# Optimization experiments

Hardware: AMD Instinct MI355X
Metric: run time of the kernel (lower is better)

Reference implementation:

```python
import jax, jax.numpy as jnp
import numpy as np

NS = (50000, 12500, 3125, 800, 200)   # mesh vertex counts per hierarchy level
CS = (3, 16, 32, 64, 128)             # in_channels + out_channels per level
S = 9       # spiral length
K = 4       # nnz per row of pooling transforms
LATENT = 128
B = 32


def setup_inputs() -> dict:
    key = jax.random.key(0)
    ks = iter(jax.random.split(key, 80))
    inp = {"x": jax.random.normal(next(ks), (B, NS[0], 3), jnp.float32)}
    for l in range(4):
        inp["spiral%d" % l] = jax.random.randint(next(ks), (NS[l], S), 0, NS[l], dtype=jnp.int32)
        # down_transform[l]: sparse (NS[l+1], NS[l])
        inp["down_rows%d" % l] = jnp.repeat(jnp.arange(NS[l + 1], dtype=jnp.int32), K)
        inp["down_cols%d" % l] = jax.random.randint(next(ks), (NS[l + 1] * K,), 0, NS[l], dtype=jnp.int32)
        inp["down_vals%d" % l] = jnp.full((NS[l + 1] * K,), 1.0 / K, jnp.float32)
        # up_transform[l]: sparse (NS[l], NS[l+1])
        inp["up_rows%d" % l] = jnp.repeat(jnp.arange(NS[l], dtype=jnp.int32), K)
        inp["up_cols%d" % l] = jax.random.randint(next(ks), (NS[l] * K,), 0, NS[l + 1], dtype=jnp.int32)
        inp["up_vals%d" % l] = jnp.full((NS[l] * K,), 1.0 / K, jnp.float32)
        # encoder SpiralConv weights: Linear(C_in*S -> C_out), stored (in, out)
        inp["enW%d" % l] = jax.random.normal(next(ks), (CS[l] * S, CS[l + 1]), jnp.float32) * 0.05
        inp["enb%d" % l] = jnp.zeros((CS[l + 1],), jnp.float32)
    inp["muW"] = jax.random.normal(next(ks), (NS[4] * CS[4], LATENT), jnp.float32) * 0.02
    inp["mub"] = jnp.zeros((LATENT,), jnp.float32)
    inp["deW0"] = jax.random.normal(next(ks), (LATENT, NS[4] * CS[4]), jnp.float32) * 0.02
    inp["deb0"] = jnp.zeros((NS[4] * CS[4],), jnp.float32)
    dcin = (CS[4], CS[4], CS[3], CS[2])
    dcout = (CS[4], CS[3], CS[2], CS[1])
    for i in range(4):
        inp["dW%d" % i] = jax.random.normal(next(ks), (dcin[i] * S, dcout[i]), jnp.float32) * 0.05
        inp["db%d" % i] = jnp.zeros((dcout[i],), jnp.float32)
    inp["outW"] = jax.random.normal(next(ks), (CS[1] * S, 3), jnp.float32) * 0.05
    inp["outb"] = jnp.zeros((3,), jnp.float32)
    return inp


def _sconv(x, idx, W, b):
    # x: (B, N, C); idx: (N, S) -> gather spiral neighbors, flatten, dense Linear
    g = x[:, idx.reshape(-1), :].reshape(x.shape[0], idx.shape[0], -1)  # (B, N, S*C)
    return g @ W + b


def _pool(x, rows, cols, vals, M):
    # sparse (M, N) transform applied along vertex dim: index_select + scale + scatter_add
    out = jnp.zeros((x.shape[0], M, x.shape[2]), x.dtype)
    return out.at[:, rows].add(x[:, cols] * vals[None, :, None])


def _forward(x, spirals, downs, ups, enWs, enbs, muW, mub, deW0, deb0, dWs, dbs, outW, outb):
    # encode: (SpiralConv -> ELU -> Pool) x4
    h = x
    for l in range(4):
        h = jax.nn.elu(_sconv(h, spirals[l], enWs[l], enbs[l]))
        h = _pool(h, downs[l][0], downs[l][1], downs[l][2], NS[l + 1])
    h = h.reshape(h.shape[0], -1)  # (B, num_vert * C_last)
    mu = jax.nn.sigmoid(h @ muW + mub)  # is_vae=False path: sigmoid(mu), logvar=None
    z = mu
    # decode: Linear -> (Pool -> SpiralConv -> ELU) x4 -> SpiralConv
    d = (z @ deW0 + deb0).reshape(-1, NS[4], CS[4])
    for i in range(4):
        l = 3 - i
        d = _pool(d, ups[l][0], ups[l][1], ups[l][2], NS[l])
        d = jax.nn.elu(_sconv(d, spirals[l], dWs[i], dbs[i]))
    out = _sconv(d, spirals[0], outW, outb)
    return out, z, mu


def reference(x, spiral0, down_rows0, down_cols0, down_vals0, up_rows0, up_cols0, up_vals0, enW0, enb0, spiral1, down_rows1, down_cols1, down_vals1, up_rows1, up_cols1, up_vals1, enW1, enb1, spiral2, down_rows2, down_cols2, down_vals2, up_rows2, up_cols2, up_vals2, enW2, enb2, spiral3, down_rows3, down_cols3, down_vals3, up_rows3, up_cols3, up_vals3, enW3, enb3, muW, mub, deW0, deb0, dW0, db0, dW1, db1, dW2, db2, dW3, db3, outW, outb):
    spirals = [spiral0, spiral1, spiral2, spiral3]
    downs = [(down_rows0, down_cols0, down_vals0), (down_rows1, down_cols1, down_vals1), (down_rows2, down_cols2, down_vals2), (down_rows3, down_cols3, down_vals3)]
    ups = [(up_rows0, up_cols0, up_vals0), (up_rows1, up_cols1, up_vals1), (up_rows2, up_cols2, up_vals2), (up_rows3, up_cols3, up_vals3)]
    return _forward(x, spirals, downs, ups, [enW0, enW1, enW2, enW3], [enb0, enb1, enb2, enb3], muW, mub, deW0, deb0, [dW0, dW1, dW2, dW3], [db0, db1, db2, db3], outW, outb)
```

## Files before the change

### kernel.cpp

```cpp
#include <hip/hip_runtime.h>
#include <hip/hip_bf16.h>
#include <math.h>

#define NS0 50000
#define NS1 12500
#define NS2 3125
#define NS3 800
#define NS4 200
#define BATCH 32
#define SLEN 9

typedef __hip_bfloat16 bf16;
typedef __attribute__((ext_vector_type(8))) short short8_t;
typedef __attribute__((ext_vector_type(4))) float f32x4;

struct WcvAll {
    const float* W[9];
    bf16* dst[9];
    int K[9], CO[9], KP[9];
    int off[10];
};

__global__ void __launch_bounds__(256)
wconv_all_kernel(WcvAll p)
{
    int gid = blockIdx.x * 256 + threadIdx.x;
    if (gid >= p.off[9]) return;
    int seg = 0;
    #pragma unroll
    for (int s = 1; s < 9; ++s) seg += (gid >= p.off[s]);
    int local = gid - p.off[seg];
    int NKK = p.KP[seg] >> 5;
    int jj   = local & 7;
    int g8   = local >> 3;
    int lane = g8 & 63;
    int blk  = g8 >> 6;
    int kk   = blk % NKK;
    int cb   = blk / NKK;
    int col0 = lane & 15, kh = lane >> 4;
    int co = cb * 16 + col0;
    int k  = kk * 32 + kh * 8 + jj;
    float v = (k < p.K[seg] && co < p.CO[seg]) ? p.W[seg][k * p.CO[seg] + co] : 0.f;
    p.dst[seg][local] = __float2bfloat16(v);
}

__global__ void __launch_bounds__(256)
xpose_in_kernel(const float* __restrict__ x, bf16* __restrict__ xT)
{
    __shared__ short ldsb[256 * 3];
    const int t = threadIdx.x;
    const int n0 = blockIdx.x * 8;
    const int b = t >> 3, v = t & 7;
    const float* src = x + ((size_t)b * NS0 + n0 + v) * 3;
    short* d = &ldsb[(v * 32 + b) * 3];
    d[0] = __bfloat16_as_short(__float2bfloat16(src[0]));
    d[1] = __bfloat16_as_short(__float2bfloat16(src[1]));
    d[2] = __bfloat16_as_short(__float2bfloat16(src[2]));
    __syncthreads();
    short* dst = (short*)xT + ((size_t)n0 * 32 + t) * 3;
    dst[0] = ldsb[t * 3 + 0];
    dst[1] = ldsb[t * 3 + 1];
    dst[2] = ldsb[t * 3 + 2];
}

__global__ void __launch_bounds__(256)
xpose_out_kernel(const float* __restrict__ vm, float* __restrict__ out)
{
    __shared__ float ldsf[256 * 3];
    const int t = threadIdx.x;
    const int n0 = blockIdx.x * 8;
    const float* src = vm + ((size_t)n0 * 32 + t) * 3;
    ldsf[t * 3 + 0] = src[0];
    ldsf[t * 3 + 1] = src[1];
    ldsf[t * 3 + 2] = src[2];
    __syncthreads();
    const int b = t >> 3, v = t & 7;
    float* dst = out + ((size_t)b * NS0 + n0 + v) * 3;
    const float* s = &ldsf[(v * 32 + b) * 3];
    dst[0] = s[0];
    dst[1] = s[1];
    dst[2] = s[2];
}

__global__ void __launch_bounds__(256)
sconv_enc0(const bf16* __restrict__ xT, const int* __restrict__ idx,
           const bf16* __restrict__ Wfrag, const float* __restrict__ bias,
           bf16* __restrict__ y)
{
    __shared__ short lds[64 * 40];
    const int t = threadIdx.x;
    const int n0 = blockIdx.x * 2;

    for (int e = t; e < 64 * 5; e += 256) {
        int r = e / 5, k = 27 + (e - r * 5);
        lds[r * 40 + k] = 0;
    }
    for (int e = t; e < 2 * 9 * 32; e += 256) {
        int v = e / 288;
        int rem = e - v * 288;
        int s = rem >> 5, b = rem & 31;
        int j = idx[(n0 + v) * 9 + s];
        const short* src = (const short*)(xT + (size_t)j * 96 + b * 3);
        short* dst = &lds[(v * 32 + b) * 40 + s * 3];
        dst[0] = src[0];
        dst[1] = src[1];
        dst[2] = src[2];
    }
    __syncthreads();

    const int w = t >> 6, lane = t & 63;
    const int col0 = lane & 15, kh = lane >> 4;
    const int rbase = w * 16;
    float bv = bias[col0];
    f32x4 acc = (f32x4){bv, bv, bv, bv};
    short8_t bfr = *(const short8_t*)(Wfrag + (size_t)lane * 8);
    short8_t afr = *(const short8_t*)&lds[(rbase + col0) * 40 + kh * 8];
    acc = __builtin_amdgcn_mfma_f32_16x16x32_bf16(afr, bfr, acc, 0, 0, 0);
    #pragma unroll
    for (int i = 0; i < 4; ++i) {
        int rl = rbase + kh * 4 + i;
        float v = acc[i];
        v = v > 0.f ? v : expm1f(v);
        y[((size_t)n0 * 32 + rl) * 16 + col0] = __float2bfloat16(v);
    }
}

template<int CIN, int COUT, int COP, int ACT, int NN, typename TOUT>
__global__ void
__launch_bounds__(256, (((9 * CIN + 31) / 32 * 32 / 32) <= 9) ? 4 : 2)
sconv_vm(const bf16* __restrict__ x, const int* __restrict__ idx,
         const bf16* __restrict__ Wfrag, const float* __restrict__ bias,
         TOUT* __restrict__ y)
{
    constexpr int KP  = (9 * CIN + 31) / 32 * 32;
    constexpr int NKK = KP / 32;
    constexpr int NCB = COP / 16;
    constexpr int CH  = (NKK <= 9) ? NKK : 6;
    constexpr int NCHUNK = NKK / CH;
    constexpr int NBUF = (NCHUNK > 1) ? 2 : 1;

    const int t = threadIdx.x, w = t >> 6, lane = t & 63;
    const int n = blockIdx.x * 4 + w;
    if (n >= NN) return;
    const int col0 = lane & 15, kh = lane >> 4;

    int jn[9];
    #pragma unroll
    for (int s = 0; s < 9; ++s) jn[s] = idx[n * 9 + s];

    f32x4 acc[2][NCB];
    #pragma unroll
    for (int cb = 0; cb < NCB; ++cb) {
        int col = cb * 16 + col0;
        float bv = (col < COUT) ? bias[col] : 0.f;
        acc[0][cb] = (f32x4){bv, bv, bv, bv};
        acc[1][cb] = (f32x4){bv, bv, bv, bv};
    }

    const short8_t z8 = {0, 0, 0, 0, 0, 0, 0, 0};
    auto loadA = [&](int kk, short8_t& a0, short8_t& a1) {
        a0 = z8; a1 = z8;
        if constexpr (CIN == 16) {
            const int hi = kh >> 1;
            const int ch = (kh & 1) * 8;
            if (kk < 4) {
                int j = hi ? jn[2 * kk + 1] : jn[2 * kk];
                const bf16* base = x + (size_t)j * 512 + ch;
                a0 = *(const short8_t*)(base + col0 * 16);
                a1 = *(const short8_t*)(base + 256 + col0 * 16);
            } else if (!hi) {
                int j = jn[8];
                const bf16* base = x + (size_t)j * 512 + ch;
                a0 = *(const short8_t*)(base + col0 * 16);
                a1 = *(const short8_t*)(base + 256 + col0 * 16);
            }
        } else {
            constexpr int SPK = CIN / 32;
            const int j = jn[kk / SPK];
            const int ch = (kk % SPK) * 32 + kh * 8;
            const bf16* base = x + (size_t)j * (32 * CIN) + ch;
            a0 = *(const short8_t*)(base + col0 * CIN);
            a1 = *(const short8_t*)(base + (16 + col0) * CIN);
        }
    };

    short8_t bufA[NBUF][2 * CH];
    #pragma unroll
    for (int q = 0; q < CH; ++q)
        loadA(q, bufA[0][2 * q], bufA[0][2 * q + 1]);

    #pragma unroll
    for (int c = 0; c < NCHUNK; ++c) {
        const int cur = (NBUF > 1) ? (c & 1) : 0;
        if (c + 1 < NCHUNK) {
            const int nxt = (NBUF > 1) ? ((c + 1) & 1) : 0;
            #pragma unroll
            for (int q = 0; q < CH; ++q)
                loadA((c + 1) * CH + q, bufA[nxt][2 * q], bufA[nxt][2 * q + 1]);
        }
        #pragma unroll
        for (int q = 0; q < CH; ++q) {
            const int kk = c * CH + q;
            #pragma unroll
            for (int cb = 0; cb < NCB; ++cb) {
                short8_t bfr = *(const short8_t*)(Wfrag + ((size_t)(cb * NKK + kk) * 64 + lane) * 8);
                acc[0][cb] = __builtin_amdgcn_mfma_f32_16x16x32_bf16(bufA[cur][2 * q],     bfr, acc[0][cb], 0, 0, 0);
                acc[1][cb] = __builtin_amdgcn_mfma_f32_16x16x32_bf16(bufA[cur][2 * q + 1], bfr, acc[1][cb], 0, 0, 0);
            }
        }
    }

    #pragma unroll
    for (int f = 0; f < 2; ++f) {
        #pragma unroll
        for (int cb = 0; cb < NCB; ++cb) {
            int col = cb * 16 + col0;
            if (col < COUT) {
                #pragma unroll
                for (int i = 0; i < 4; ++i) {
                    int b = f * 16 + kh * 4 + i;
                    float v = acc[f][cb][i];
                    if (ACT) v = v > 0.f ? v : expm1f(v);
                    TOUT* dst = &y[((size_t)n * 32 + b) * COUT + col];
                    if constexpr (__is_same(TOUT, float)) *dst = v;
                    else *dst = __float2bfloat16(v);
                }
            }
        }
    }
}

template<int C8>
__global__ void __launch_bounds__(256)
pool_vm(const bf16* __restrict__ x, const int* __restrict__ cols,
        const float* __restrict__ vals, bf16* __restrict__ y, int M)
{
    constexpr int BC8 = 32 * C8;
    int tid = blockIdx.x * 256 + threadIdx.x;
    if (tid >= M * BC8) return;
    int m = tid / BC8;
    int e = tid - m * BC8;
    const uint4* xv = (const uint4*)x;
    float acc[8];
    #pragma unroll
    for (int q = 0; q < 8; ++q) acc[q] = 0.f;
    #pragma unroll
    for (int j = 0; j < 4; ++j) {
        int col = cols[m * 4 + j];
        float v = vals[m * 4 + j];
        uint4 u = xv[(size_t)col * BC8 + e];
        const bf16* hh = (const bf16*)&u;
        #pragma unroll
        for (int q = 0; q < 8; ++q)
            acc[q] = fmaf(v, __bfloat162float(hh[q]), acc[q]);
    }
    uint4 o;
    bf16* oh = (bf16*)&o;
    #pragma unroll
    for (int q = 0; q < 8; ++q) oh[q] = __float2bfloat16(acc[q]);
    ((uint4*)y)[(size_t)m * BC8 + e] = o;
}

__global__ void __launch_bounds__(256)
mu_partial_kernel(const bf16* __restrict__ h, const float* __restrict__ W,
                  float* __restrict__ partial)
{
    __shared__ float hs[4096];
    const int t = threadIdx.x;
    const int nb = blockIdx.x;
    const bf16* hb = h + (size_t)nb * 4096;
    for (int e = t; e < 512; e += 256) {
        short8_t v = *(const short8_t*)(hb + e * 8);
        #pragma unroll
        for (int q = 0; q < 8; ++q)
            hs[e * 8 + q] = __bfloat162float(((const bf16*)&v)[q]);
    }
    __syncthreads();
    const int co = t & 127;
    const int bh = t >> 7;
    float acc[16];
    #pragma unroll
    for (int i = 0; i < 16; ++i) acc[i] = 0.f;
    const int k0 = nb * 128;
    for (int k = 0; k < 128; ++k) {
        float wv = W[(size_t)(k0 + k) * 128 + co];
        #pragma unroll
        for (int i = 0; i < 16; ++i)
            acc[i] = fmaf(hs[(bh * 16 + i) * 128 + k], wv, acc[i]);
    }
    float* pb = partial + (size_t)nb * 4096;
    #pragma unroll
    for (int i = 0; i < 16; ++i)
        pb[(bh * 16 + i) * 128 + co] = acc[i];
}

__global__ void __launch_bounds__(256)
mu_reduce_kernel(const float* __restrict__ partial, const float* __restrict__ bias,
                 float* __restrict__ z, float* __restrict__ out_z,
                 float* __restrict__ out_mu)
{
    const int i = blockIdx.x * 256 + threadIdx.x;
    const int co = i & 127;
    float a0 = 0.f, a1 = 0.f, a2 = 0.f, a3 = 0.f;
    #pragma unroll 4
    for (int c = 0; c < 200; c += 4) {
        a0 += partial[(size_t)c * 4096 + i];
        a1 += partial[(size_t)(c + 1) * 4096 + i];
        a2 += partial[(size_t)(c + 2) * 4096 + i];
        a3 += partial[(size_t)(c + 3) * 4096 + i];
    }
    float acc = (a0 + a1) + (a2 + a3) + bias[co];
    float m = 1.f / (1.f + expf(-acc));
    z[i] = m;
    out_z[i] = m;
    out_mu[i] = m;
}

__global__ void __launch_bounds__(256)
de0_kernel(const float* __restrict__ z, const float* __restrict__ W,
           const float* __restrict__ bias, bf16* __restrict__ d)
{
    __shared__ float zs[BATCH * 128];
    const int t = threadIdx.x;
    for (int e = t; e < BATCH * 128; e += 256) zs[e] = z[e];
    __syncthreads();
    const int j = blockIdx.x * 256 + t;
    float bj = bias[j];
    float acc[BATCH];
    #pragma unroll
    for (int b = 0; b < BATCH; ++b) acc[b] = bj;
    for (int k = 0; k < 128; ++k) {
        float w = W[k * 25600 + j];
        #pragma unroll
        for (int b = 0; b < BATCH; ++b)
            acc[b] = fmaf(zs[b * 128 + k], w, acc[b]);
    }
    const int nn = j >> 7, c = j & 127;
    #pragma unroll
    for (int b = 0; b < BATCH; ++b)
        d[(size_t)nn * 4096 + b * 128 + c] = __float2bfloat16(acc[b]);
}

extern "C" void kernel_launch(void* const* d_in, const int* in_sizes, int n_in,
                              void* d_out, int out_size, void* d_ws, size_t ws_size,
                              hipStream_t stream)
{
    const float* x = (const float*)d_in[0];
    const int*   sp[4];
    const int*   dn_cols[4];
    const float* dn_vals[4];
    const int*   up_cols[4];
    const float* up_vals[4];
    const float* enW[4];
    const float* enb[4];
    for (int l = 0; l < 4; ++l) {
        int base = 1 + 9 * l;
        sp[l]      = (const int*)d_in[base + 0];
        dn_cols[l] = (const int*)d_in[base + 2];
        dn_vals[l] = (const float*)d_in[base + 3];
        up_cols[l] = (const int*)d_in[base + 5];
        up_vals[l] = (const float*)d_in[base + 6];
        enW[l]     = (const float*)d_in[base + 7];
        enb[l]     = (const float*)d_in[base + 8];
    }
    const float* muW  = (const float*)d_in[37];
    const float* mub  = (const float*)d_in[38];
    const float* deW0 = (const float*)d_in[39];
    const float* deb0 = (const float*)d_in[40];
    const float* dW[4]  = { (const float*)d_in[41], (const float*)d_in[43],
                            (const float*)d_in[45], (const float*)d_in[47] };
    const float* db[4]  = { (const float*)d_in[42], (const float*)d_in[44],
                            (const float*)d_in[46], (const float*)d_in[48] };
    const float* outW = (const float*)d_in[49];
    const float* outb = (const float*)d_in[50];

    char* ws = (char*)d_ws;
    bf16*  A  = (bf16*)ws;
    bf16*  Bb = (bf16*)(ws + 51200000);
    bf16*  xT = (bf16*)(ws + 51200000);
    float* outVM = (float*)(ws + 51200000);
    float* Z  = (float*)(ws + 153600000);
    bf16*  wEN0 = (bf16*)(ws + 153600000 + 16384);
    bf16*  wOUT = wEN0 + 512;

    float* outF   = (float*)d_out;
    float* out_z  = outF + 4800000;
    float* out_mu = outF + 4804096;

    bf16*  wsc  = (bf16*)d_out;
    bf16*  wEN1 = wsc;
    bf16*  wEN2 = wsc + 5120;
    bf16*  wEN3 = wsc + 23552;
    bf16*  wDW0 = wsc + 97280;
    bf16*  wDW1 = wsc + 244736;
    bf16*  wDW2 = wsc + 318464;
    bf16*  wDW3 = wsc + 336896;
    float* muPart = outF + 1000000;

    WcvAll wp;
    const float* srcs[9] = {enW[0], enW[1], enW[2], enW[3], dW[0], dW[1], dW[2], dW[3], outW};
    bf16* dsts[9] = {wEN0, wEN1, wEN2, wEN3, wDW0, wDW1, wDW2, wDW3, wOUT};
    int Ks[9]   = {27, 144, 288, 576, 1152, 1152, 576, 288, 144};
    int COs[9]  = {16, 32, 64, 128, 128, 64, 32, 16, 3};
    int KPs[9]  = {32, 160, 288, 576, 1152, 1152, 576, 288, 160};
    int COPs[9] = {16, 32, 64, 128, 128, 64, 32, 16, 16};
    int off = 0;
    for (int s = 0; s < 9; ++s) {
        wp.W[s] = srcs[s]; wp.dst[s] = dsts[s];
        wp.K[s] = Ks[s]; wp.CO[s] = COs[s]; wp.KP[s] = KPs[s];
        wp.off[s] = off; off += COPs[s] * KPs[s];
    }
    wp.off[9] = off;
    auto cdiv = [](int a, int b) { return (a + b - 1) / b; };
    wconv_all_kernel<<<cdiv(off, 256), 256, 0, stream>>>(wp);

    xpose_in_kernel<<<NS0 / 8, 256, 0, stream>>>(x, xT);

    sconv_enc0<<<NS0 / 2, 256, 0, stream>>>(xT, sp[0], wEN0, enb[0], A);
    pool_vm<2><<<cdiv(NS1 * 64, 256), 256, 0, stream>>>(A, dn_cols[0], dn_vals[0], Bb, NS1);
    sconv_vm<16, 32, 32, 1, NS1, bf16><<<cdiv(NS1, 4), 256, 0, stream>>>(Bb, sp[1], wEN1, enb[1], A);
    pool_vm<4><<<cdiv(NS2 * 128, 256), 256, 0, stream>>>(A, dn_cols[1], dn_vals[1], Bb, NS2);
    sconv_vm<32, 64, 64, 1, NS2, bf16><<<cdiv(NS2, 4), 256, 0, stream>>>(Bb, sp[2], wEN2, enb[2], A);
    pool_vm<8><<<cdiv(NS3 * 256, 256), 256, 0, stream>>>(A, dn_cols[2], dn_vals[2], Bb, NS3);
    sconv_vm<64, 128, 128, 1, NS3, bf16><<<cdiv(NS3, 4), 256, 0, stream>>>(Bb, sp[3], wEN3, enb[3], A);
    pool_vm<16><<<cdiv(NS4 * 512, 256), 256, 0, stream>>>(A, dn_cols[3], dn_vals[3], Bb, NS4);

    mu_partial_kernel<<<200, 256, 0, stream>>>(Bb, muW, muPart);
    mu_reduce_kernel<<<16, 256, 0, stream>>>(muPart, mub, Z, out_z, out_mu);
    de0_kernel<<<25600 / 256, 256, 0, stream>>>(Z, deW0, deb0, A);

    pool_vm<16><<<cdiv(NS3 * 512, 256), 256, 0, stream>>>(A, up_cols[3], up_vals[3], Bb, NS3);
    sconv_vm<128, 128, 128, 1, NS3, bf16><<<cdiv(NS3, 4), 256, 0, stream>>>(Bb, sp[3], wDW0, db[0], A);
    pool_vm<16><<<cdiv(NS2 * 512, 256), 256, 0, stream>>>(A, up_cols[2], up_vals[2], Bb, NS2);
    sconv_vm<128, 64, 64, 1, NS2, bf16><<<cdiv(NS2, 4), 256, 0, stream>>>(Bb, sp[2], wDW1, db[1], A);
    pool_vm<8><<<cdiv(NS1 * 256, 256), 256, 0, stream>>>(A, up_cols[1], up_vals[1], Bb, NS1);
    sconv_vm<64, 32, 32, 1, NS1, bf16><<<cdiv(NS1, 4), 256, 0, stream>>>(Bb, sp[1], wDW2, db[2], A);
    pool_vm<4><<<cdiv(NS0 * 128, 256), 256, 0, stream>>>(A, up_cols[0], up_vals[0], Bb, NS0);
    sconv_vm<32, 16, 16, 1, NS0, bf16><<<cdiv(NS0, 4), 256, 0, stream>>>(Bb, sp[0], wDW3, db[3], A);

    sconv_vm<16, 3, 16, 0, NS0, float><<<cdiv(NS0, 4), 256, 0, stream>>>(A, sp[0], wOUT, outb, outVM);
    xpose_out_kernel<<<NS0 / 8, 256, 0, stream>>>(outVM, outF);
}
```

Before: 756.7 us.

## Fuse output transpose into final spiral conv and split sconv into small/big variants

The final 3-channel spiral conv now writes directly in batch-major layout through an LDS transpose, removing the separate transpose kernel and its intermediate buffer. The generic sconv kernel is split in two. The small-input variant loads all A fragments before issuing MFMAs. The large-input variant loads each 9-step chunk and then computes, behind a scheduling barrier, replacing the previous double-buffered prefetch. This trades load/compute overlap for lower register pressure and simpler scheduling.

New measurement: 746.0 us. No clear change (-1.4%).

```diff
diff --git a/kernel.cpp b/kernel.cpp
--- a/kernel.cpp
+++ b/kernel.cpp
@@ -64,25 +64,6 @@
 }
 
 __global__ void __launch_bounds__(256)
-xpose_out_kernel(const float* __restrict__ vm, float* __restrict__ out)
-{
-    __shared__ float ldsf[256 * 3];
-    const int t = threadIdx.x;
-    const int n0 = blockIdx.x * 8;
-    const float* src = vm + ((size_t)n0 * 32 + t) * 3;
-    ldsf[t * 3 + 0] = src[0];
-    ldsf[t * 3 + 1] = src[1];
-    ldsf[t * 3 + 2] = src[2];
-    __syncthreads();
-    const int b = t >> 3, v = t & 7;
-    float* dst = out + ((size_t)b * NS0 + n0 + v) * 3;
-    const float* s = &ldsf[(v * 32 + b) * 3];
-    dst[0] = s[0];
-    dst[1] = s[1];
-    dst[2] = s[2];
-}
-
-__global__ void __launch_bounds__(256)
 sconv_enc0(const bf16* __restrict__ xT, const int* __restrict__ idx,
            const bf16* __restrict__ Wfrag, const float* __restrict__ bias,
            bf16* __restrict__ y)
@@ -125,19 +106,17 @@
     }
 }
 
-template<int CIN, int COUT, int COP, int ACT, int NN, typename TOUT>
-__global__ void
-__launch_bounds__(256, (((9 * CIN + 31) / 32 * 32 / 32) <= 9) ? 4 : 2)
-sconv_vm(const bf16* __restrict__ x, const int* __restrict__ idx,
-         const bf16* __restrict__ Wfrag, const float* __restrict__ bias,
-         TOUT* __restrict__ y)
+template<int CIN, int COUT, int COP, int ACT, int NN, int XPOSE, typename TOUT>
+__global__ void __launch_bounds__(256, 4)
+sconv_small(const bf16* __restrict__ x, const int* __restrict__ idx,
+            const bf16* __restrict__ Wfrag, const float* __restrict__ bias,
+            TOUT* __restrict__ y)
 {
     constexpr int KP  = (9 * CIN + 31) / 32 * 32;
     constexpr int NKK = KP / 32;
     constexpr int NCB = COP / 16;
-    constexpr int CH  = (NKK <= 9) ? NKK : 6;
-    constexpr int NCHUNK = NKK / CH;
-    constexpr int NBUF = (NCHUNK > 1) ? 2 : 1;
+    constexpr int XD  = XPOSE ? 4 : 1;
+    __shared__ float xls[XD][32][3];
 
     const int t = threadIdx.x, w = t >> 6, lane = t & 63;
     const int n = blockIdx.x * 4 + w;
@@ -158,8 +137,10 @@
     }
 
     const short8_t z8 = {0, 0, 0, 0, 0, 0, 0, 0};
-    auto loadA = [&](int kk, short8_t& a0, short8_t& a1) {
-        a0 = z8; a1 = z8;
+    short8_t fa[2 * NKK];
+    #pragma unroll
+    for (int kk = 0; kk < NKK; ++kk) {
+        short8_t a0 = z8, a1 = z8;
         if constexpr (CIN == 16) {
             const int hi = kh >> 1;
             const int ch = (kh & 1) * 8;
@@ -175,37 +156,113 @@
                 a1 = *(const short8_t*)(base + 256 + col0 * 16);
             }
         } else {
-            constexpr int SPK = CIN / 32;
+            const int j = jn[kk];
+            const bf16* base = x + (size_t)j * 1024 + kh * 8;
+            a0 = *(const short8_t*)(base + col0 * 32);
+            a1 = *(const short8_t*)(base + (16 + col0) * 32);
+        }
+        fa[2 * kk] = a0;
+        fa[2 * kk + 1] = a1;
+    }
+    __builtin_amdgcn_sched_barrier(0);
+
+    #pragma unroll
+    for (int kk = 0; kk < NKK; ++kk) {
+        #pragma unroll
+        for (int cb = 0; cb < NCB; ++cb) {
+            short8_t bfr = *(const short8_t*)(Wfrag + ((size_t)(cb * NKK + kk) * 64 + lane) * 8);
+            acc[0][cb] = __builtin_amdgcn_mfma_f32_16x16x32_bf16(fa[2 * kk],     bfr, acc[0][cb], 0, 0, 0);
+            acc[1][cb] = __builtin_amdgcn_mfma_f32_16x16x32_bf16(fa[2 * kk + 1], bfr, acc[1][cb], 0, 0, 0);
+        }
+    }
+
+    if constexpr (XPOSE) {
+        if (col0 < 3) {
+            #pragma unroll
+            for (int f = 0; f < 2; ++f)
+                #pragma unroll
+                for (int i = 0; i < 4; ++i)
+                    xls[w][f * 16 + kh * 4 + i][col0] = acc[f][0][i];
+        }
+        __syncthreads();
+        const int n0 = blockIdx.x * 4;
+        for (int e = t; e < 384; e += 256) {
+            int b = e / 12, rem = e - b * 12;
+            int v = rem / 3, c = rem - v * 3;
+            y[((size_t)b * NN + n0 + v) * 3 + c] = xls[v][b][c];
+        }
+    } else {
+        #pragma unroll
+        for (int f = 0; f < 2; ++f) {
+            #pragma unroll
+            for (int cb = 0; cb < NCB; ++cb) {
+                int col = cb * 16 + col0;
+                if (col < COUT) {
+                    #pragma unroll
+                    for (int i = 0; i < 4; ++i) {
+                        int b = f * 16 + kh * 4 + i;
+                        float v = acc[f][cb][i];
+                        if (ACT) v = v > 0.f ? v : expm1f(v);
+                        y[((size_t)n * 32 + b) * COUT + col] = __float2bfloat16(v);
+                    }
+                }
+            }
+        }
+    }
+}
+
+template<int CIN, int COUT, int COP, int ACT, int NN>
+__global__ void __launch_bounds__(256, (COP >= 128 || CIN >= 128) ? 2 : 4)
+sconv_big(const bf16* __restrict__ x, const int* __restrict__ idx,
+          const bf16* __restrict__ Wfrag, const float* __restrict__ bias,
+          bf16* __restrict__ y)
+{
+    constexpr int KP  = 9 * CIN;
+    constexpr int NKK = KP / 32;
+    constexpr int NCB = COP / 16;
+    constexpr int CH  = 9;
+    constexpr int NCHUNK = NKK / CH;
+
+    const int t = threadIdx.x, w = t >> 6, lane = t & 63;
+    const int n = blockIdx.x * 4 + w;
+    if (n >= NN) return;
+    const int col0 = lane & 15, kh = lane >> 4;
+
+    int jn[9];
+    #pragma unroll
+    for (int s = 0; s < 9; ++s) jn[s] = idx[n * 9 + s];
+
+    f32x4 acc[2][NCB];
+    #pragma unroll
+    for (int cb = 0; cb < NCB; ++cb) {
+        int col = cb * 16 + col0;
+        float bv = (col < COUT) ? bias[col] : 0.f;
+        acc[0][cb] = (f32x4){bv, bv, bv, bv};
+        acc[1][cb] = (f32x4){bv, bv, bv, bv};
+    }
+
+    constexpr int SPK = CIN / 32;
+    short8_t fa[2 * CH];
+    #pragma unroll
+    for (int c = 0; c < NCHUNK; ++c) {
+        #pragma unroll
+        for (int q = 0; q < CH; ++q) {
+            const int kk = c * CH + q;
             const int j = jn[kk / SPK];
             const int ch = (kk % SPK) * 32 + kh * 8;
             const bf16* base = x + (size_t)j * (32 * CIN) + ch;
-            a0 = *(const short8_t*)(base + col0 * CIN);
-            a1 = *(const short8_t*)(base + (16 + col0) * CIN);
-        }
-    };
-
-    short8_t bufA[NBUF][2 * CH];
-    #pragma unroll
-    for (int q = 0; q < CH; ++q)
-        loadA(q, bufA[0][2 * q], bufA[0][2 * q + 1]);
-
-    #pragma unroll
-    for (int c = 0; c < NCHUNK; ++c) {
-        const int cur = (NBUF > 1) ? (c & 1) : 0;
-        if (c + 1 < NCHUNK) {
-            const int nxt = (NBUF > 1) ? ((c + 1) & 1) : 0;
-            #pragma unroll
-            for (int q = 0; q < CH; ++q)
-                loadA((c + 1) * CH + q, bufA[nxt][2 * q], bufA[nxt][2 * q + 1]);
-        }
+            fa[2 * q]     = *(const short8_t*)(base + col0 * CIN);
+            fa[2 * q + 1] = *(const short8_t*)(base + (16 + col0) * CIN);
+        }
+        __builtin_amdgcn_sched_barrier(0);
         #pragma unroll
         for (int q = 0; q < CH; ++q) {
             const int kk = c * CH + q;
             #pragma unroll
             for (int cb = 0; cb < NCB; ++cb) {
                 short8_t bfr = *(const short8_t*)(Wfrag + ((size_t)(cb * NKK + kk) * 64 + lane) * 8);
-                acc[0][cb] = __builtin_amdgcn_mfma_f32_16x16x32_bf16(bufA[cur][2 * q],     bfr, acc[0][cb], 0, 0, 0);
-                acc[1][cb] = __builtin_amdgcn_mfma_f32_16x16x32_bf16(bufA[cur][2 * q + 1], bfr, acc[1][cb], 0, 0, 0);
+                acc[0][cb] = __builtin_amdgcn_mfma_f32_16x16x32_bf16(fa[2 * q],     bfr, acc[0][cb], 0, 0, 0);
+                acc[1][cb] = __builtin_amdgcn_mfma_f32_16x16x32_bf16(fa[2 * q + 1], bfr, acc[1][cb], 0, 0, 0);
             }
         }
     }
@@ -221,9 +278,7 @@
                     int b = f * 16 + kh * 4 + i;
                     float v = acc[f][cb][i];
                     if (ACT) v = v > 0.f ? v : expm1f(v);
-                    TOUT* dst = &y[((size_t)n * 32 + b) * COUT + col];
-                    if constexpr (__is_same(TOUT, float)) *dst = v;
-                    else *dst = __float2bfloat16(v);
+                    y[((size_t)n * 32 + b) * COUT + col] = __float2bfloat16(v);
                 }
             }
         }
@@ -378,7 +433,6 @@
     bf16*  A  = (bf16*)ws;
     bf16*  Bb = (bf16*)(ws + 51200000);
     bf16*  xT = (bf16*)(ws + 51200000);
-    float* outVM = (float*)(ws + 51200000);
     float* Z  = (float*)(ws + 153600000);
     bf16*  wEN0 = (bf16*)(ws + 153600000 + 16384);
     bf16*  wOUT = wEN0 + 512;
@@ -418,11 +472,11 @@
 
     sconv_enc0<<<NS0 / 2, 256, 0, stream>>>(xT, sp[0], wEN0, enb[0], A);
     pool_vm<2><<<cdiv(NS1 * 64, 256), 256, 0, stream>>>(A, dn_cols[0], dn_vals[0], Bb, NS1);
-    sconv_vm<16, 32, 32, 1, NS1, bf16><<<cdiv(NS1, 4), 256, 0, stream>>>(Bb, sp[1], wEN1, enb[1], A);
+    sconv_small<16, 32, 32, 1, NS1, 0, bf16><<<cdiv(NS1, 4), 256, 0, stream>>>(Bb, sp[1], wEN1, enb[1], A);
     pool_vm<4><<<cdiv(NS2 * 128, 256), 256, 0, stream>>>(A, dn_cols[1], dn_vals[1], Bb, NS2);
-    sconv_vm<32, 64, 64, 1, NS2, bf16><<<cdiv(NS2, 4), 256, 0, stream>>>(Bb, sp[2], wEN2, enb[2], A);
+    sconv_small<32, 64, 64, 1, NS2, 0, bf16><<<cdiv(NS2, 4), 256, 0, stream>>>(Bb, sp[2], wEN2, enb[2], A);
     pool_vm<8><<<cdiv(NS3 * 256, 256), 256, 0, stream>>>(A, dn_cols[2], dn_vals[2], Bb, NS3);
-    sconv_vm<64, 128, 128, 1, NS3, bf16><<<cdiv(NS3, 4), 256, 0, stream>>>(Bb, sp[3], wEN3, enb[3], A);
+    sconv_big<64, 128, 128, 1, NS3><<<cdiv(NS3, 4), 256, 0, stream>>>(Bb, sp[3], wEN3, enb[3], A);
     pool_vm<16><<<cdiv(NS4 * 512, 256), 256, 0, stream>>>(A, dn_cols[3], dn_vals[3], Bb, NS4);
 
     mu_partial_kernel<<<200, 256, 0, stream>>>(Bb, muW, muPart);
@@ -430,14 +484,13 @@
     de0_kernel<<<25600 / 256, 256, 0, stream>>>(Z, deW0, deb0, A);
 
     pool_vm<16><<<cdiv(NS3 * 512, 256), 256, 0, stream>>>(A, up_cols[3], up_vals[3], Bb, NS3);
-    sconv_vm<128, 128, 128, 1, NS3, bf16><<<cdiv(NS3, 4), 256, 0, stream>>>(Bb, sp[3], wDW0, db[0], A);
+    sconv_big<128, 128, 128, 1, NS3><<<cdiv(NS3, 4), 256, 0, stream>>>(Bb, sp[3], wDW0, db[0], A);
     pool_vm<16><<<cdiv(NS2 * 512, 256), 256, 0, stream>>>(A, up_cols[2], up_vals[2], Bb, NS2);
-    sconv_vm<128, 64, 64, 1, NS2, bf16><<<cdiv(NS2, 4), 256, 0, stream>>>(Bb, sp[2], wDW1, db[1], A);
+    sconv_big<128, 64, 64, 1, NS2><<<cdiv(NS2, 4), 256, 0, stream>>>(Bb, sp[2], wDW1, db[1], A);
     pool_vm<8><<<cdiv(NS1 * 256, 256), 256, 0, stream>>>(A, up_cols[1], up_vals[1], Bb, NS1);
-    sconv_vm<64, 32, 32, 1, NS1, bf16><<<cdiv(NS1, 4), 256, 0, stream>>>(Bb, sp[1], wDW2, db[2], A);
+    sconv_big<64, 32, 32, 1, NS1><<<cdiv(NS1, 4), 256, 0, stream>>>(Bb, sp[1], wDW2, db[2], A);
     pool_vm<4><<<cdiv(NS0 * 128, 256), 256, 0, stream>>>(A, up_cols[0], up_vals[0], Bb, NS0);
-    sconv_vm<32, 16, 16, 1, NS0, bf16><<<cdiv(NS0, 4), 256, 0, stream>>>(Bb, sp[0], wDW3, db[3], A);
-
-    sconv_vm<16, 3, 16, 0, NS0, float><<<cdiv(NS0, 4), 256, 0, stream>>>(A, sp[0], wOUT, outb, outVM);
-    xpose_out_kernel<<<NS0 / 8, 256, 0, stream>>>(outVM, outF);
-}
+    sconv_small<32, 16, 16, 1, NS0, 0, bf16><<<cdiv(NS0, 4), 256, 0, stream>>>(Bb, sp[0], wDW3, db[3], A);
+
+    sconv_small<16, 3, 16, 0, NS0, 1, float><<<cdiv(NS0, 4), 256, 0, stream>>>(A, sp[0], wOUT, outb, outF);
+}
```
